# Kernel optimization log

Hardware: AMD Instinct MI355X
Metric: run time of the kernel (lower is better)

The kernel has to match this reference:

```python
import jax, jax.numpy as jnp
import numpy as np
import math

B, T, C = 4, 2048, 1024
NH = 16
HD = C // NH


def setup_inputs() -> dict:
    key = jax.random.key(0)
    ks = jax.random.split(key, 10)
    s = 0.02
    x = jax.random.normal(ks[0], (B, T, C), dtype=jnp.float32)
    W_qkv = jax.random.normal(ks[1], (C, 3 * C), dtype=jnp.float32) * s
    b_qkv = jnp.zeros((3 * C,), dtype=jnp.float32)
    W_proj = jax.random.normal(ks[2], (C, C), dtype=jnp.float32) * s
    b_proj = jnp.zeros((C,), dtype=jnp.float32)
    asym_mean, asym_std = 1.0, 0.7
    q_scale = jax.random.normal(ks[3], (NH, HD), dtype=jnp.float32) * asym_std + asym_mean
    q_bias = jax.random.normal(ks[4], (NH, HD), dtype=jnp.float32) * asym_std + asym_mean
    k_scale = jax.random.normal(ks[5], (NH, HD), dtype=jnp.float32) * asym_std + asym_mean
    k_bias = jax.random.normal(ks[6], (NH, HD), dtype=jnp.float32) * asym_std + asym_mean
    return {"x": x, "W_qkv": W_qkv, "b_qkv": b_qkv, "W_proj": W_proj,
            "b_proj": b_proj, "q_scale": q_scale, "q_bias": q_bias,
            "k_scale": k_scale, "k_bias": k_bias}


def reference(x, W_qkv, b_qkv, W_proj, b_proj, q_scale, q_bias, k_scale, k_bias):
    Bx, Tx, Cx = x.shape
    qkv = x @ W_qkv + b_qkv                       # [B,T,3C]
    q, k, v = jnp.split(qkv, 3, axis=-1)
    # [B,T,C] -> [B,NH,T,HD]
    reshape = lambda t: t.reshape(Bx, Tx, NH, HD).transpose(0, 2, 1, 3)
    q, k, v = reshape(q), reshape(k), reshape(v)
    # per-head affine scaling of Q/K
    q = q * q_scale[None, :, None, :] + q_bias[None, :, None, :]
    k = k * k_scale[None, :, None, :] + k_bias[None, :, None, :]
    scores = jnp.einsum('bhqd,bhkd->bhqk', q, k) / math.sqrt(HD)  # [B,NH,T,T]
    causal = jnp.tril(jnp.ones((Tx, Tx), dtype=bool))
    scores = jnp.where(causal[None, None], scores, -jnp.inf)
    att = jax.nn.softmax(scores, axis=-1)
    y = jnp.einsum('bhqk,bhkd->bhqd', att, v)     # [B,NH,T,HD]
    y = y.transpose(0, 2, 1, 3).reshape(Bx, Tx, Cx)
    return y @ W_proj + b_proj
```

## Files before the change

kernel.cpp:

```cpp
#include <hip/hip_runtime.h>
#include <hip/hip_bf16.h>

typedef unsigned short u16;
typedef __attribute__((ext_vector_type(8))) short short8;
typedef __attribute__((ext_vector_type(4))) float floatx4;

#define B_SZ 4
#define T_SZ 2048
#define C_SZ 1024
#define NH_SZ 16
#define HD_SZ 64
#define M_TOT 8192
#define K_DIM 1024

#define QSCALE 0.1803368801111204f

#define OFF_XB   ((size_t)16)
#define OFF_WQT  (OFF_XB + 8388608)
#define OFF_WPT  (OFF_WQT + 3145728)
#define OFF_PB   (OFF_WPT + 1048576)
#define OFF_Q    (OFF_PB + 8192)
#define OFF_K    (OFF_Q + 8388608)
#define OFF_V    (OFF_K + 8388608)
#define OFF_Y    (OFF_V + 8388608)
#define PB_BQKV  0
#define PB_BPROJ 3072
#define PB_QSC   4096
#define PB_QBI   5120
#define PB_KSC   6144
#define PB_KBI   7168

__device__ __forceinline__ float bf2f(u16 u) {
    return __uint_as_float(((unsigned)u) << 16);
}
__device__ __forceinline__ u16 f2bf(float f) {
    unsigned x = __float_as_uint(f);
    unsigned r = (x + 0x7fffu + ((x >> 16) & 1u)) >> 16;
    return (u16)r;
}
__device__ __forceinline__ u16 f2bf_fast(float f) {
    return (u16)((__float_as_uint(f) + 0x8000u) >> 16);
}
__device__ __forceinline__ unsigned cvt_pk_bf16(float lo, float hi) {
    unsigned r;
    asm("v_cvt_pk_bf16_f32 %0, %1, %2" : "=v"(r) : "v"(lo), "v"(hi));
    return r;
}
__device__ __forceinline__ void gl_lds16(const u16* g, u16* l) {
    __builtin_amdgcn_global_load_lds(
        (const __attribute__((address_space(1))) void*)g,
        (__attribute__((address_space(3))) void*)l, 16, 0, 0);
}
__device__ __forceinline__ int detect_isf(const u16* xx, int lane) {
    float v0 = fabsf(bf2f(xx[lane * 2]));
    float v1 = fabsf(bf2f(xx[lane * 2 + 1]));
    int b0 = (v0 > 1024.0f) || (v0 != 0.0f && v0 < 9.5367431640625e-7f);
    int b1 = (v1 > 1024.0f) || (v1 != 0.0f && v1 < 9.5367431640625e-7f);
    unsigned long long ba = __ballot(b0), bb = __ballot(b1);
    return (__popcll(ba) + __popcll(bb)) > 8;
}

__global__ __launch_bounds__(256) void prep_k(
        const void* __restrict__ x,
        const void* __restrict__ Wqkv, const void* __restrict__ Wproj,
        const void* __restrict__ bqkv, const void* __restrict__ bproj,
        const void* __restrict__ qsc, const void* __restrict__ qbi,
        const void* __restrict__ ksc, const void* __restrict__ kbi,
        u16* __restrict__ xb, u16* __restrict__ Wt_qkv,
        u16* __restrict__ Wt_proj, u16* __restrict__ pb,
        int* __restrict__ flag) {
    __shared__ u16 t[32][33];
    const int blk = blockIdx.x;
    const int isf = detect_isf((const u16*)x, threadIdx.x & 63);
    if (blk == 0 && threadIdx.x == 0) flag[0] = isf;
    if (blk < 8192) {
        const int i = blk * 256 + threadIdx.x;
        if (isf) {
            const float4 v = ((const float4*)x)[i];
            ushort4 o;
            o.x = f2bf(v.x); o.y = f2bf(v.y); o.z = f2bf(v.z); o.w = f2bf(v.w);
            ((ushort4*)xb)[i] = o;
        } else {
            ((ushort4*)xb)[i] = ((const ushort4*)x)[i];
        }
        return;
    }
    if (blk < 8200) {
        const int i4 = (blk - 8192) * 256 + threadIdx.x;
        if (i4 >= 2048) return;
        const int e = i4 * 4;
        const void* src; int off;
        if (e < 3072)      { src = bqkv;  off = e; }
        else if (e < 4096) { src = bproj; off = e - 3072; }
        else if (e < 5120) { src = qsc;   off = e - 4096; }
        else if (e < 6144) { src = qbi;   off = e - 5120; }
        else if (e < 7168) { src = ksc;   off = e - 6144; }
        else               { src = kbi;   off = e - 7168; }
        ushort4 o;
        if (isf) {
            const float4 v = *(const float4*)((const float*)src + off);
            o.x = f2bf(v.x); o.y = f2bf(v.y); o.z = f2bf(v.z); o.w = f2bf(v.w);
        } else {
            o = *(const ushort4*)((const u16*)src + off);
        }
        *(ushort4*)&pb[e] = o;
        return;
    }
    const void* in; u16* out; int R, C, idx;
    if (blk < 11272) { idx = blk - 8200;  in = Wqkv;  out = Wt_qkv;  R = 1024; C = 3072; }
    else             { idx = blk - 11272; in = Wproj; out = Wt_proj; R = 1024; C = 1024; }
    const int nbx = C >> 5;
    const int c0 = (idx % nbx) * 32, r0 = (idx / nbx) * 32;
    const int tx = threadIdx.x & 31, ty = threadIdx.x >> 5;
    for (int i = 0; i < 4; i++) {
        int r = ty + i * 8;
        size_t gi = (size_t)(r0 + r) * C + c0 + tx;
        t[r][tx] = isf ? f2bf(((const float*)in)[gi]) : ((const u16*)in)[gi];
    }
    __syncthreads();
    for (int i = 0; i < 4; i++) {
        int cr = ty + i * 8;
        out[(size_t)(c0 + cr) * R + r0 + tx] = t[tx][cr];
    }
}

#define QG_BM 128
#define QG_BN 192
#define QG_NT 16

__global__ __launch_bounds__(512, 4) void qkv_gemm(
        const u16* __restrict__ X, const u16* __restrict__ Wt,
        const u16* __restrict__ pb,
        u16* __restrict__ Qb, u16* __restrict__ Kb, u16* __restrict__ Vb) {
    __shared__ __align__(16) u16 As[2][QG_BM * 64];
    __shared__ __align__(16) u16 Bs[2][QG_BN * 64];
    const int bm = blockIdx.y * QG_BM, bn = blockIdx.x * QG_BN;
    const int tid = threadIdx.x;
    const int lane = tid & 63, w = tid >> 6;
    const int quad = lane >> 4, l16 = lane & 15;
    const int wm = (w >> 2) * 64;
    const int wn = (w & 3) * 48;
    const int lrow = lane >> 3;
    const int lcol = ((lane & 7) ^ lrow) * 8;
    const int sl0 = ((0 + quad) ^ (l16 & 7)) * 8;
    const int sl1 = ((4 + quad) ^ (l16 & 7)) * 8;

#define QG_STAGE(slot, kt) do {                                                  \
        const int k0_ = (kt) * 64;                                               \
        _Pragma("unroll")                                                        \
        for (int j = 0; j < 2; j++) {                                            \
            const int rb = w * 16 + j * 8;                                       \
            gl_lds16(&X[(size_t)(bm + rb + lrow) * K_DIM + k0_ + lcol],          \
                     &As[slot][rb * 64]);                                        \
        }                                                                        \
        _Pragma("unroll")                                                        \
        for (int j = 0; j < 3; j++) {                                            \
            const int rb = w * 24 + j * 8;                                       \
            gl_lds16(&Wt[(size_t)(bn + rb + lrow) * K_DIM + k0_ + lcol],         \
                     &Bs[slot][rb * 64]);                                        \
        }                                                                        \
    } while (0)

    floatx4 acc[4][3];
#pragma unroll
    for (int mi = 0; mi < 4; mi++)
#pragma unroll
        for (int ni = 0; ni < 3; ni++) acc[mi][ni] = 0.f;

    QG_STAGE(0, 0);
    QG_STAGE(1, 1);
    asm volatile("s_waitcnt vmcnt(5)" ::: "memory");
    __builtin_amdgcn_s_barrier();

    for (int t = 0; t < QG_NT; ++t) {
        const int cur = t & 1;
        const u16* as = As[cur];
        const u16* bs = Bs[cur];
        short8 a[4], b[3];
#pragma unroll
        for (int mi = 0; mi < 4; mi++)
            a[mi] = *(const short8*)&as[(wm + mi * 16 + l16) * 64 + sl0];
#pragma unroll
        for (int ni = 0; ni < 3; ni++)
            b[ni] = *(const short8*)&bs[(wn + ni * 16 + l16) * 64 + sl0];
        __builtin_amdgcn_s_setprio(1);
#pragma unroll
        for (int mi = 0; mi < 4; mi++)
#pragma unroll
            for (int ni = 0; ni < 3; ni++)
                acc[mi][ni] = __builtin_amdgcn_mfma_f32_16x16x32_bf16(
                    a[mi], b[ni], acc[mi][ni], 0, 0, 0);
        __builtin_amdgcn_s_setprio(0);
#pragma unroll
        for (int mi = 0; mi < 4; mi++)
            a[mi] = *(const short8*)&as[(wm + mi * 16 + l16) * 64 + sl1];
#pragma unroll
        for (int ni = 0; ni < 3; ni++)
            b[ni] = *(const short8*)&bs[(wn + ni * 16 + l16) * 64 + sl1];
        asm volatile("s_waitcnt lgkmcnt(0)" ::: "memory");
        __builtin_amdgcn_s_barrier();
        if (t < QG_NT - 1) {
            const int tn = (t + 2 < QG_NT) ? t + 2 : QG_NT - 1;
            QG_STAGE(cur, tn);
        }
        __builtin_amdgcn_s_setprio(1);
#pragma unroll
        for (int mi = 0; mi < 4; mi++)
#pragma unroll
            for (int ni = 0; ni < 3; ni++)
                acc[mi][ni] = __builtin_amdgcn_mfma_f32_16x16x32_bf16(
                    a[mi], b[ni], acc[mi][ni], 0, 0, 0);
        __builtin_amdgcn_s_setprio(0);
        asm volatile("s_waitcnt vmcnt(5)" ::: "memory");
        __builtin_amdgcn_s_barrier();
    }
#undef QG_STAGE

    const int bb = bm >> 11;
    const int tbase = bm & 2047;
#pragma unroll
    for (int ni = 0; ni < 3; ni++) {
        const int col = bn + wn + ni * 16 + l16;
        const int sec = col >> 10;
        const int cmod = col & 1023;
        const int h = cmod >> 6, d = cmod & 63;
        const float bv = bf2f(pb[PB_BQKV + col]);
        if (sec == 2) {
#pragma unroll
            for (int mi = 0; mi < 4; mi++) {
                const int t0 = tbase + wm + mi * 16 + quad * 4;
                ushort4 pk;
                pk.x = f2bf(acc[mi][ni][0] + bv);
                pk.y = f2bf(acc[mi][ni][1] + bv);
                pk.z = f2bf(acc[mi][ni][2] + bv);
                pk.w = f2bf(acc[mi][ni][3] + bv);
                *(ushort4*)&Vb[(((size_t)(bb * NH_SZ + h)) * HD_SZ + d) * T_SZ + t0] = pk;
            }
        } else {
            float sA, sB;
            if (sec == 0) {
                sA = bf2f(pb[PB_QSC + h * 64 + d]) * QSCALE;
                sB = bf2f(pb[PB_QBI + h * 64 + d]) * QSCALE;
            } else {
                sA = bf2f(pb[PB_KSC + h * 64 + d]);
                sB = bf2f(pb[PB_KBI + h * 64 + d]);
            }
            u16* dstbuf = (sec == 0) ? Qb : Kb;
#pragma unroll
            for (int mi = 0; mi < 4; mi++)
#pragma unroll
                for (int r = 0; r < 4; r++) {
                    const int tt = tbase + wm + mi * 16 + quad * 4 + r;
                    float v = (acc[mi][ni][r] + bv) * sA + sB;
                    dstbuf[(((size_t)(bb * NH_SZ + h)) * T_SZ + tt) * HD_SZ + d] = f2bf(v);
                }
        }
    }
}

__global__ __launch_bounds__(512, 6) void attn_k(const u16* __restrict__ Qb,
                                                 const u16* __restrict__ Kb,
                                                 const u16* __restrict__ Vtg,
                                                 u16* __restrict__ Y) {
    __shared__ __align__(16) u16 Ks[2][64 * 64];
    __shared__ __align__(16) u16 Vs[2][64 * 64];
    __shared__ __align__(16) u16 Ps[8 * 16 * 72];
    const int blk = blockIdx.x;
    const int head = blk & 63;
    const int qt = 15 - (blk >> 6);
    const int b = head >> 4, h = head & 15;
    const int tid = threadIdx.x, lane = tid & 63, w = tid >> 6;
    const int quad = lane >> 4, l16 = lane & 15;
    const size_t qk_off = (size_t)head * (T_SZ * HD_SZ);
    const size_t v_off = (size_t)head * (HD_SZ * T_SZ);
    u16* psw = &Ps[w * 1152];
    const int lr = lane >> 3;
    const int lc = ((lane & 7) ^ lr) * 8;
    const int sl0 = ((quad) ^ (l16 & 7)) * 8;
    const int sl1 = ((4 + quad) ^ (l16 & 7)) * 8;

    short8 ones;
    for (int j = 0; j < 8; j++) ones[j] = (short)0x3F80;

    const int q0 = qt * 128;
    const int rbase = q0 + w * 16;
    const int q = rbase + l16;
    const int nt = (q0 >> 6) + 2;

    const short8 aq0 = *(const short8*)&Qb[qk_off + (size_t)q * HD_SZ + quad * 8];
    const short8 aq1 = *(const short8*)&Qb[qk_off + (size_t)q * HD_SZ + 32 + quad * 8];

    floatx4 o[4];
    for (int mi = 0; mi < 4; mi++) o[mi] = 0.f;
    float m_run = -1e30f, l_run = 0.f;

    gl_lds16(&Kb[qk_off + (size_t)(w * 8 + lr) * HD_SZ + lc], &Ks[0][w * 512]);
    gl_lds16(&Vtg[v_off + (size_t)(w * 8 + lr) * T_SZ + lc], &Vs[0][w * 512]);

    for (int t = 0; t < nt; ++t) {
        const int cur = t & 1;
        const int k0 = t * 64;
        if (t + 1 < nt) {
            const int kn = k0 + 64;
            gl_lds16(&Kb[qk_off + (size_t)(kn + w * 8 + lr) * HD_SZ + lc],
                     &Ks[cur ^ 1][w * 512]);
            gl_lds16(&Vtg[v_off + (size_t)(w * 8 + lr) * T_SZ + kn + lc],
                     &Vs[cur ^ 1][w * 512]);
            asm volatile("s_waitcnt vmcnt(2)" ::: "memory");
        } else {
            asm volatile("s_waitcnt vmcnt(0)" ::: "memory");
        }
        __builtin_amdgcn_s_barrier();

        if (k0 <= rbase + 15) {
            const u16* ks = Ks[cur];
            const u16* vs = Vs[cur];
            floatx4 s[4];
            for (int ni = 0; ni < 4; ni++) s[ni] = 0.f;
            __builtin_amdgcn_s_setprio(1);
            for (int ni = 0; ni < 4; ni++)
                s[ni] = __builtin_amdgcn_mfma_f32_16x16x32_bf16(
                    *(const short8*)&ks[(ni * 16 + l16) * 64 + sl0], aq0, s[ni], 0, 0, 0);
            for (int ni = 0; ni < 4; ni++)
                s[ni] = __builtin_amdgcn_mfma_f32_16x16x32_bf16(
                    *(const short8*)&ks[(ni * 16 + l16) * 64 + sl1], aq1, s[ni], 0, 0, 0);
            __builtin_amdgcn_s_setprio(0);

            if (k0 + 63 > rbase) {
                for (int ni = 0; ni < 4; ni++)
                    for (int r = 0; r < 4; r++) {
                        int key = k0 + ni * 16 + quad * 4 + r;
                        if (key > q) s[ni][r] = -1e30f;
                    }
            }

            float t0 = fmaxf(fmaxf(s[0][0], s[0][1]), s[0][2]);
            float t1 = fmaxf(fmaxf(s[0][3], s[1][0]), s[1][1]);
            float t2 = fmaxf(fmaxf(s[1][2], s[1][3]), s[2][0]);
            float t3 = fmaxf(fmaxf(s[2][1], s[2][2]), s[2][3]);
            float t4 = fmaxf(fmaxf(s[3][0], s[3][1]), s[3][2]);
            float mx = fmaxf(fmaxf(fmaxf(t0, t1), fmaxf(t2, t3)),
                             fmaxf(t4, s[3][3]));
            mx = fmaxf(mx, __shfl_xor(mx, 16, 64));
            mx = fmaxf(mx, __shfl_xor(mx, 32, 64));

            if (!__all(mx <= m_run + 8.0f)) {
                const float mnew = fmaxf(m_run, mx);
                const float alpha = exp2f(m_run - mnew);
                m_run = mnew;
                for (int mi = 0; mi < 4; mi++) o[mi] *= alpha;
                l_run *= alpha;
            }
            for (int ni = 0; ni < 4; ni++)
                for (int r = 0; r < 4; r++)
                    s[ni][r] = exp2f(s[ni][r] - m_run);

            for (int ni = 0; ni < 4; ni++) {
                uint2 pp;
                pp.x = cvt_pk_bf16(s[ni][0], s[ni][1]);
                pp.y = cvt_pk_bf16(s[ni][2], s[ni][3]);
                *(uint2*)&psw[l16 * 72 + ni * 16 + quad * 4] = pp;
            }

            floatx4 s4 = 0.f;
            __builtin_amdgcn_s_setprio(1);
            for (int kk = 0; kk < 64; kk += 32) {
                short8 pfr = *(const short8*)&psw[l16 * 72 + kk + quad * 8];
                const int vsl = (kk == 0) ? sl0 : sl1;
                s4 = __builtin_amdgcn_mfma_f32_16x16x32_bf16(ones, pfr, s4, 0, 0, 0);
                for (int mi = 0; mi < 4; mi++) {
                    short8 vfr = *(const short8*)&vs[(mi * 16 + l16) * 64 + vsl];
                    o[mi] = __builtin_amdgcn_mfma_f32_16x16x32_bf16(vfr, pfr, o[mi], 0, 0, 0);
                }
            }
            __builtin_amdgcn_s_setprio(0);
            l_run += s4[0];
        }
        asm volatile("s_waitcnt lgkmcnt(0)" ::: "memory");
        __builtin_amdgcn_s_barrier();
    }

    const float inv = 1.0f / l_run;
    u16* yrow = &Y[(((size_t)b * T_SZ + q) * NH_SZ + h) * HD_SZ];
    for (int mi = 0; mi < 4; mi++) {
        uint2 pk2;
        pk2.x = cvt_pk_bf16(o[mi][0] * inv, o[mi][1] * inv);
        pk2.y = cvt_pk_bf16(o[mi][2] * inv, o[mi][3] * inv);
        *(uint2*)&yrow[mi * 16 + quad * 4] = pk2;
    }
}

#define PG_NT 16

__global__ __launch_bounds__(512, 4) void proj_gemm(const u16* __restrict__ Yin,
                                                    const u16* __restrict__ Wt,
                                                    const u16* __restrict__ pb,
                                                    void* __restrict__ out,
                                                    const int* __restrict__ flag) {
    __shared__ __align__(16) u16 As[2][128 * 64];
    __shared__ __align__(16) u16 Bs[2][128 * 64];
    const int isf = flag[0];
    const int bm = blockIdx.y * 128, bn = blockIdx.x * 128;
    const int tid = threadIdx.x;
    const int lane = tid & 63, w = tid >> 6;
    const int quad = lane >> 4, l16 = lane & 15;
    const int wm = (w & 3) * 32, wn = (w >> 2) * 64;
    const int lrow = lane >> 3;
    const int lcol = ((lane & 7) ^ lrow) * 8;
    const int sl0 = ((0 + quad) ^ (l16 & 7)) * 8;
    const int sl1 = ((4 + quad) ^ (l16 & 7)) * 8;

#define PG_STAGE(slot, kt) do {                                                  \
        const int k0_ = (kt) * 64;                                               \
        _Pragma("unroll")                                                        \
        for (int j = 0; j < 2; j++) {                                            \
            const int rb = w * 16 + j * 8;                                       \
            gl_lds16(&Yin[(size_t)(bm + rb + lrow) * K_DIM + k0_ + lcol],        \
                     &As[slot][rb * 64]);                                        \
            gl_lds16(&Wt[(size_t)(bn + rb + lrow) * K_DIM + k0_ + lcol],         \
                     &Bs[slot][rb * 64]);                                        \
        }                                                                        \
    } while (0)

    floatx4 acc[2][4];
#pragma unroll
    for (int mi = 0; mi < 2; mi++)
#pragma unroll
        for (int ni = 0; ni < 4; ni++) acc[mi][ni] = 0.f;

    PG_STAGE(0, 0);
    PG_STAGE(1, 1);
    asm volatile("s_waitcnt vmcnt(4)" ::: "memory");
    __builtin_amdgcn_s_barrier();

    for (int t = 0; t < PG_NT; ++t) {
        const int cur = t & 1;
        const u16* as = As[cur];
        const u16* bs = Bs[cur];
        short8 a[2], b[4];
#pragma unroll
        for (int mi = 0; mi < 2; mi++)
            a[mi] = *(const short8*)&as[(wm + mi * 16 + l16) * 64 + sl0];
#pragma unroll
        for (int ni = 0; ni < 4; ni++)
            b[ni] = *(const short8*)&bs[(wn + ni * 16 + l16) * 64 + sl0];
        __builtin_amdgcn_s_setprio(1);
#pragma unroll
        for (int mi = 0; mi < 2; mi++)
#pragma unroll
            for (int ni = 0; ni < 4; ni++)
                acc[mi][ni] = __builtin_amdgcn_mfma_f32_16x16x32_bf16(
                    a[mi], b[ni], acc[mi][ni], 0, 0, 0);
        __builtin_amdgcn_s_setprio(0);
#pragma unroll
        for (int mi = 0; mi < 2; mi++)
            a[mi] = *(const short8*)&as[(wm + mi * 16 + l16) * 64 + sl1];
#pragma unroll
        for (int ni = 0; ni < 4; ni++)
            b[ni] = *(const short8*)&bs[(wn + ni * 16 + l16) * 64 + sl1];
        asm volatile("s_waitcnt lgkmcnt(0)" ::: "memory");
        __builtin_amdgcn_s_barrier();
        if (t < PG_NT - 1) {
            const int tn = (t + 2 < PG_NT) ? t + 2 : PG_NT - 1;
            PG_STAGE(cur, tn);
        }
        __builtin_amdgcn_s_setprio(1);
#pragma unroll
        for (int mi = 0; mi < 2; mi++)
#pragma unroll
            for (int ni = 0; ni < 4; ni++)
                acc[mi][ni] = __builtin_amdgcn_mfma_f32_16x16x32_bf16(
                    a[mi], b[ni], acc[mi][ni], 0, 0, 0);
        __builtin_amdgcn_s_setprio(0);
        asm volatile("s_waitcnt vmcnt(4)" ::: "memory");
        __builtin_amdgcn_s_barrier();
    }
#undef PG_STAGE

    for (int mi = 0; mi < 2; mi++) {
        for (int ni = 0; ni < 4; ni++) {
            const int col = bn + wn + ni * 16 + l16;
            const float bv = bf2f(pb[PB_BPROJ + col]);
            for (int r = 0; r < 4; r++) {
                const int row = bm + wm + mi * 16 + quad * 4 + r;
                const float v = acc[mi][ni][r] + bv;
                if (isf) ((float*)out)[(size_t)row * C_SZ + col] = v;
                else     ((u16*)out)[(size_t)row * C_SZ + col] = f2bf(v);
            }
        }
    }
}

extern "C" void kernel_launch(void* const* d_in, const int* in_sizes, int n_in,
                              void* d_out, int out_size, void* d_ws, size_t ws_size,
                              hipStream_t stream) {
    const void* x     = d_in[0];
    const void* Wqkv  = d_in[1];
    const void* bqkv  = d_in[2];
    const void* Wproj = d_in[3];
    const void* bproj = d_in[4];
    const void* qsc   = d_in[5];
    const void* qbi   = d_in[6];
    const void* ksc   = d_in[7];
    const void* kbi   = d_in[8];

    u16* ws = (u16*)d_ws;
    int* flag    = (int*)d_ws;
    u16* xb      = ws + OFF_XB;
    u16* Wt_qkv  = ws + OFF_WQT;
    u16* Wt_proj = ws + OFF_WPT;
    u16* pb      = ws + OFF_PB;
    u16* Qb      = ws + OFF_Q;
    u16* Kb      = ws + OFF_K;
    u16* Vb      = ws + OFF_V;
    u16* Yb      = ws + OFF_Y;

    prep_k<<<12296, 256, 0, stream>>>(x, Wqkv, Wproj, bqkv, bproj,
                                      qsc, qbi, ksc, kbi,
                                      xb, Wt_qkv, Wt_proj, pb, flag);
    qkv_gemm<<<dim3(16, 64), 512, 0, stream>>>(xb, Wt_qkv, pb, Qb, Kb, Vb);
    attn_k<<<dim3(1024), 512, 0, stream>>>(Qb, Kb, Vb, Yb);
    proj_gemm<<<dim3(8, 64), 512, 0, stream>>>(Yb, Wt_proj, pb, d_out, flag);
}
```

Baseline: 270.2 us.

## Enlarge QKV GEMM tile to 256x192 with 64x96 per-wave subtiles

The QKV projection GEMM block tile grows from 128x192 to 256x192. Each of the 8 waves now computes a 64x96 subtile, so there are twice as many accumulators per wave, and the grid in M is halved. The inner loop is split into four MFMA phases with extra barriers and LDS fragment reloads. This raises arithmetic intensity per LDS load and halves global reads of the weight tile, at the cost of more registers, lower occupancy (launch bounds 2) and fewer blocks (512) to fill the CUs.

```diff
diff --git a/kernel.cpp b/kernel.cpp
--- a/kernel.cpp
+++ b/kernel.cpp
@@ -124,11 +124,11 @@
     }
 }
 
-#define QG_BM 128
+#define QG_BM 256
 #define QG_BN 192
 #define QG_NT 16
 
-__global__ __launch_bounds__(512, 4) void qkv_gemm(
+__global__ __launch_bounds__(512, 2) void qkv_gemm(
         const u16* __restrict__ X, const u16* __restrict__ Wt,
         const u16* __restrict__ pb,
         u16* __restrict__ Qb, u16* __restrict__ Kb, u16* __restrict__ Vb) {
@@ -138,8 +138,8 @@
     const int tid = threadIdx.x;
     const int lane = tid & 63, w = tid >> 6;
     const int quad = lane >> 4, l16 = lane & 15;
-    const int wm = (w >> 2) * 64;
-    const int wn = (w & 3) * 48;
+    const int wm = (w & 3) * 64;
+    const int wn = (w >> 2) * 96;
     const int lrow = lane >> 3;
     const int lcol = ((lane & 7) ^ lrow) * 8;
     const int sl0 = ((0 + quad) ^ (l16 & 7)) * 8;
@@ -148,8 +148,8 @@
 #define QG_STAGE(slot, kt) do {                                                  \
         const int k0_ = (kt) * 64;                                               \
         _Pragma("unroll")                                                        \
-        for (int j = 0; j < 2; j++) {                                            \
-            const int rb = w * 16 + j * 8;                                       \
+        for (int j = 0; j < 4; j++) {                                            \
+            const int rb = w * 32 + j * 8;                                       \
             gl_lds16(&X[(size_t)(bm + rb + lrow) * K_DIM + k0_ + lcol],          \
                      &As[slot][rb * 64]);                                        \
         }                                                                        \
@@ -161,15 +161,15 @@
         }                                                                        \
     } while (0)
 
-    floatx4 acc[4][3];
+    floatx4 acc[4][6];
 #pragma unroll
     for (int mi = 0; mi < 4; mi++)
 #pragma unroll
-        for (int ni = 0; ni < 3; ni++) acc[mi][ni] = 0.f;
+        for (int ni = 0; ni < 6; ni++) acc[mi][ni] = 0.f;
 
     QG_STAGE(0, 0);
     QG_STAGE(1, 1);
-    asm volatile("s_waitcnt vmcnt(5)" ::: "memory");
+    asm volatile("s_waitcnt vmcnt(7)" ::: "memory");
     __builtin_amdgcn_s_barrier();
 
     for (int t = 0; t < QG_NT; ++t) {
@@ -177,12 +177,15 @@
         const u16* as = As[cur];
         const u16* bs = Bs[cur];
         short8 a[4], b[3];
+
 #pragma unroll
         for (int mi = 0; mi < 4; mi++)
             a[mi] = *(const short8*)&as[(wm + mi * 16 + l16) * 64 + sl0];
 #pragma unroll
         for (int ni = 0; ni < 3; ni++)
             b[ni] = *(const short8*)&bs[(wn + ni * 16 + l16) * 64 + sl0];
+        __builtin_amdgcn_s_barrier();
+        asm volatile("s_waitcnt lgkmcnt(0)" ::: "memory");
         __builtin_amdgcn_s_setprio(1);
 #pragma unroll
         for (int mi = 0; mi < 4; mi++)
@@ -191,18 +194,29 @@
                 acc[mi][ni] = __builtin_amdgcn_mfma_f32_16x16x32_bf16(
                     a[mi], b[ni], acc[mi][ni], 0, 0, 0);
         __builtin_amdgcn_s_setprio(0);
+
+#pragma unroll
+        for (int ni = 0; ni < 3; ni++)
+            b[ni] = *(const short8*)&bs[(wn + (ni + 3) * 16 + l16) * 64 + sl0];
+        __builtin_amdgcn_s_barrier();
+        asm volatile("s_waitcnt lgkmcnt(0)" ::: "memory");
+        __builtin_amdgcn_s_setprio(1);
+#pragma unroll
+        for (int mi = 0; mi < 4; mi++)
+#pragma unroll
+            for (int ni = 0; ni < 3; ni++)
+                acc[mi][ni + 3] = __builtin_amdgcn_mfma_f32_16x16x32_bf16(
+                    a[mi], b[ni], acc[mi][ni + 3], 0, 0, 0);
+        __builtin_amdgcn_s_setprio(0);
+
 #pragma unroll
         for (int mi = 0; mi < 4; mi++)
             a[mi] = *(const short8*)&as[(wm + mi * 16 + l16) * 64 + sl1];
 #pragma unroll
         for (int ni = 0; ni < 3; ni++)
             b[ni] = *(const short8*)&bs[(wn + ni * 16 + l16) * 64 + sl1];
+        __builtin_amdgcn_s_barrier();
         asm volatile("s_waitcnt lgkmcnt(0)" ::: "memory");
-        __builtin_amdgcn_s_barrier();
-        if (t < QG_NT - 1) {
-            const int tn = (t + 2 < QG_NT) ? t + 2 : QG_NT - 1;
-            QG_STAGE(cur, tn);
-        }
         __builtin_amdgcn_s_setprio(1);
 #pragma unroll
         for (int mi = 0; mi < 4; mi++)
@@ -211,7 +225,25 @@
                 acc[mi][ni] = __builtin_amdgcn_mfma_f32_16x16x32_bf16(
                     a[mi], b[ni], acc[mi][ni], 0, 0, 0);
         __builtin_amdgcn_s_setprio(0);
-        asm volatile("s_waitcnt vmcnt(5)" ::: "memory");
+
+#pragma unroll
+        for (int ni = 0; ni < 3; ni++)
+            b[ni] = *(const short8*)&bs[(wn + (ni + 3) * 16 + l16) * 64 + sl1];
+        asm volatile("s_waitcnt lgkmcnt(0)" ::: "memory");
+        __builtin_amdgcn_s_barrier();
+        if (t < QG_NT - 1) {
+            const int tn = (t + 2 < QG_NT) ? t + 2 : QG_NT - 1;
+            QG_STAGE(cur, tn);
+        }
+        __builtin_amdgcn_s_setprio(1);
+#pragma unroll
+        for (int mi = 0; mi < 4; mi++)
+#pragma unroll
+            for (int ni = 0; ni < 3; ni++)
+                acc[mi][ni + 3] = __builtin_amdgcn_mfma_f32_16x16x32_bf16(
+                    a[mi], b[ni], acc[mi][ni + 3], 0, 0, 0);
+        __builtin_amdgcn_s_setprio(0);
+        asm volatile("s_waitcnt vmcnt(7)" ::: "memory");
         __builtin_amdgcn_s_barrier();
     }
 #undef QG_STAGE
@@ -219,7 +251,7 @@
     const int bb = bm >> 11;
     const int tbase = bm & 2047;
 #pragma unroll
-    for (int ni = 0; ni < 3; ni++) {
+    for (int ni = 0; ni < 6; ni++) {
         const int col = bn + wn + ni * 16 + l16;
         const int sec = col >> 10;
         const int cmod = col & 1023;
@@ -518,7 +550,7 @@
     prep_k<<<12296, 256, 0, stream>>>(x, Wqkv, Wproj, bqkv, bproj,
                                       qsc, qbi, ksc, kbi,
                                       xb, Wt_qkv, Wt_proj, pb, flag);
-    qkv_gemm<<<dim3(16, 64), 512, 0, stream>>>(xb, Wt_qkv, pb, Qb, Kb, Vb);
+    qkv_gemm<<<dim3(16, 32), 512, 0, stream>>>(xb, Wt_qkv, pb, Qb, Kb, Vb);
     attn_k<<<dim3(1024), 512, 0, stream>>>(Qb, Kb, Vb, Yb);
     proj_gemm<<<dim3(8, 64), 512, 0, stream>>>(Yb, Wt_proj, pb, d_out, flag);
 }
```

Result: slower. 295.1 us (+9.2%).
